# Kernel tuning notes

Measured on AMD Instinct MI355X. Metric: run time of the kernel, lower is better.

Reference implementation:

```python
import jax, jax.numpy as jnp
import numpy as np

N_NODES = 10000
N_EDGES = 160000
IN_DIM = 512
HID = 256
HEADS = 4
OUT_DIM = 512
NEG_SLOPE = 0.2  # PyG GATConv default


def _glorot(key, shape):
    fan_in, fan_out = shape[0], shape[-1]
    lim = jnp.sqrt(6.0 / (fan_in + fan_out))
    return jax.random.uniform(key, shape, jnp.float32, -lim, lim)


def setup_inputs() -> dict:
    key = jax.random.key(0)
    ks = jax.random.split(key, 16)
    x = jax.random.normal(ks[0], (N_NODES, IN_DIM), jnp.float32)
    edge_index = jax.random.randint(ks[1], (2, N_EDGES), 0, N_NODES, jnp.int64)
    # layer 1: GATConv(512 -> 256, heads=4, concat) -> out 1024
    W1 = _glorot(ks[2], (IN_DIM, HEADS * HID))
    att_src1 = _glorot(ks[3], (HEADS, HID))
    att_dst1 = _glorot(ks[4], (HEADS, HID))
    b1 = jnp.zeros((HEADS * HID,), jnp.float32)
    # layer 2: GATConv(1024 -> 256, heads=4, concat) -> out 1024
    W2 = _glorot(ks[5], (HEADS * HID, HEADS * HID))
    att_src2 = _glorot(ks[6], (HEADS, HID))
    att_dst2 = _glorot(ks[7], (HEADS, HID))
    b2 = jnp.zeros((HEADS * HID,), jnp.float32)
    # final fc: 1024 -> 512
    fcW = _glorot(ks[8], (HEADS * HID, OUT_DIM))
    fcb = jnp.zeros((OUT_DIM,), jnp.float32)
    return dict(x=x, edge_index=edge_index, W1=W1, att_src1=att_src1,
                att_dst1=att_dst1, b1=b1, W2=W2, att_src2=att_src2,
                att_dst2=att_dst2, b2=b2, fcW=fcW, fcb=fcb)


def gat_conv(x, src, dst, W, att_src, att_dst, bias):
    # x: [N, F_in]; src/dst: [E] (self-loops already included)
    N = x.shape[0]
    h = (x @ W).reshape(N, HEADS, HID)                       # [N, H, C]
    a_src = jnp.sum(h * att_src, axis=-1)                    # [N, H]
    a_dst = jnp.sum(h * att_dst, axis=-1)                    # [N, H]
    e = jax.nn.leaky_relu(a_src[src] + a_dst[dst], NEG_SLOPE)  # [E, H]
    # numerically stable segment softmax over destination nodes
    m = jax.ops.segment_max(e, dst, num_segments=N)          # [N, H]
    e = jnp.exp(e - m[dst])
    s = jax.ops.segment_sum(e, dst, num_segments=N)          # [N, H]
    alpha = e / (s[dst] + 1e-16)                             # [E, H]
    msg = alpha[:, :, None] * h[src]                         # [E, H, C]
    out = jax.ops.segment_sum(msg, dst, num_segments=N)      # [N, H, C]
    return out.reshape(N, HEADS * HID) + bias


def reference(x, edge_index, W1, att_src1, att_dst1, b1,
              W2, att_src2, att_dst2, b2, fcW, fcb):
    N = x.shape[0]
    loops = jnp.arange(N, dtype=edge_index.dtype)
    src = jnp.concatenate([edge_index[0], loops])  # PyG add_self_loops=True
    dst = jnp.concatenate([edge_index[1], loops])
    h = gat_conv(x, src, dst, W1, att_src1, att_dst1, b1)
    h = jax.nn.relu(h)  # dropout is identity in eval mode
    h = gat_conv(h, src, dst, W2, att_src2, att_dst2, b2)
    h = jax.nn.relu(h)
    return h @ fcW + fcb
```

## Files before the change

### kernel.cpp

```cpp
#include <hip/hip_runtime.h>
#include <hip/hip_bf16.h>

#define NN 10000
#define NE 160000
#define NET 170000
#define IN_DIM 512
#define D1 1024
#define HEADS 4
#define HID 256
#define OUT_DIM 512
#define NEG_SLOPE 0.2f

typedef __attribute__((ext_vector_type(8))) short bf16x8;
typedef __attribute__((ext_vector_type(4))) float f32x4;

__device__ inline float b2f(unsigned short b) {
    union { unsigned u; float f; } x; x.u = ((unsigned)b) << 16; return x.f;
}
__device__ inline unsigned short f2b(float f) {
    union { float f; unsigned u; } x; x.f = f;
    unsigned u = x.u;
    unsigned r = u + 0x7FFFu + ((u >> 16) & 1u);
    return (unsigned short)(r >> 16);
}
__device__ inline float lrelu(float v) { return v > 0.f ? v : NEG_SLOPE * v; }

__device__ inline bool is64(const int* ei32) {
    int acc = 0;
#pragma unroll
    for (int k = 0; k < 16; k++) acc |= ei32[2 * k + 1];
    return acc == 0;
}

__device__ inline void load_edge(const void* ei, bool f64, int e, int& s, int& d) {
    if (f64) {
        const long long* p = (const long long*)ei;
        s = (int)p[e]; d = (int)p[NE + e];
    } else {
        const int* p = (const int*)ei;
        s = p[e]; d = p[NE + e];
    }
}

__global__ void zero_kernel(int* counts, int* cursor) {
    int i = blockIdx.x * blockDim.x + threadIdx.x;
    if (i < NN) { counts[i] = 0; cursor[i] = 0; }
}

__device__ void scan_dev(const int* counts, int* indptr) {
    __shared__ int part[256];
    int t = threadIdx.x;
    int base = t * 40;
    int local[40];
    int sum = 0;
#pragma unroll
    for (int k = 0; k < 40; k++) {
        int i = base + k;
        int c = (i < NN) ? counts[i] : 0;
        local[k] = sum;
        sum += c;
    }
    part[t] = sum;
    __syncthreads();
    for (int off = 1; off < 256; off <<= 1) {
        int v = (t >= off) ? part[t - off] : 0;
        __syncthreads();
        part[t] += v;
        __syncthreads();
    }
    int excl = part[t] - sum;
#pragma unroll
    for (int k = 0; k < 40; k++) {
        int i = base + k;
        if (i < NN) indptr[i] = excl + local[k];
    }
    if (t == 255) indptr[NN] = part[255];
}

__device__ void tpose_tile(const float* __restrict__ in, unsigned short* __restrict__ out,
                           int R, int C, int bx, int by) {
    __shared__ float tile[32][33];
    int tx = threadIdx.x & 31, ty = threadIdx.x >> 5;
    int c = bx * 32 + tx;
#pragma unroll
    for (int r0 = 0; r0 < 32; r0 += 8) {
        int r = by * 32 + ty + r0;
        tile[ty + r0][tx] = in[(size_t)r * C + c];
    }
    __syncthreads();
    int oc = by * 32 + tx;
#pragma unroll
    for (int r0 = 0; r0 < 32; r0 += 8) {
        int orow = bx * 32 + ty + r0;
        out[(size_t)orow * R + oc] = f2b(tile[tx][ty + r0]);
    }
}

#define CVT_NB 5000
#define TP1_NB 512
#define TP2_NB 1024
#define TP3_NB 512
#define CNT_NB 665
__global__ __launch_bounds__(256) void setup_kernel(
    const void* ei, int* counts,
    const float* __restrict__ x, unsigned short* __restrict__ xb,
    const float* __restrict__ W1, unsigned short* __restrict__ W1t,
    const float* __restrict__ W2, unsigned short* __restrict__ W2t,
    const float* __restrict__ fcW, unsigned short* __restrict__ fcWt) {
    int b = blockIdx.x;
    if (b < CVT_NB) {
        int i = b * 256 + threadIdx.x;
        float4 v = reinterpret_cast<const float4*>(x)[i];
        ushort4 o;
        o.x = f2b(v.x); o.y = f2b(v.y); o.z = f2b(v.z); o.w = f2b(v.w);
        reinterpret_cast<ushort4*>(xb)[i] = o;
        return;
    }
    b -= CVT_NB;
    if (b < TP1_NB) { tpose_tile(W1, W1t, IN_DIM, D1, b & 31, b >> 5); return; }
    b -= TP1_NB;
    if (b < TP2_NB) { tpose_tile(W2, W2t, D1, D1, b & 31, b >> 5); return; }
    b -= TP2_NB;
    if (b < TP3_NB) { tpose_tile(fcW, fcWt, D1, OUT_DIM, b & 15, b >> 4); return; }
    b -= TP3_NB;
    int e = b * 256 + threadIdx.x;
    if (e >= NET) return;
    bool f64 = is64((const int*)ei);
    int s, d;
    if (e < NE) load_edge(ei, f64, e, s, d);
    else d = e - NE;
    atomicAdd(&counts[d], 1);
}

template<int TBM, int TBN>
__global__ __launch_bounds__(256) void gemmT(
    const unsigned short* __restrict__ A, const unsigned short* __restrict__ B,
    const float* __restrict__ bias, float* __restrict__ Cf, unsigned short* __restrict__ Cb,
    int M, int N, int K, int NB, int NWG,
    const int* __restrict__ sc_counts, int* __restrict__ sc_indptr) {
    if ((int)blockIdx.x >= NWG) { scan_dev(sc_counts, sc_indptr); return; }
    constexpr int FM = TBM / 32;
    constexpr int FN = TBN / 32;
    constexpr int AISS = TBM / 32;
    constexpr int BISS = TBN / 32;
    constexpr int ABUF = TBM * 64;
    constexpr int BBUF = TBN * 64;
    __shared__ __align__(16) unsigned short As[2 * ABUF];
    __shared__ __align__(16) unsigned short Bs[2 * BBUF];
    int t = threadIdx.x;
    int q = NWG >> 3, r = NWG & 7;
    int xcd = blockIdx.x & 7, jj = blockIdx.x >> 3;
    int wg = (xcd < r ? xcd * (q + 1) : r * (q + 1) + (xcd - r) * q) + jj;
    int row0 = (wg / NB) * TBM, col0 = (wg % NB) * TBN;

    int w = t >> 6, l = t & 63;
    int wr = w >> 1, wc = w & 1;
    f32x4 acc[FM][FN] = {};

    int srow = w * 8 + (l >> 3);
    int scs = ((l & 7) ^ (l >> 3)) * 8;
    const unsigned short* ap[AISS];
    const unsigned short* bp[BISS];
#pragma unroll
    for (int i = 0; i < AISS; i++)
        ap[i] = A + (size_t)min(row0 + i * 32 + srow, M - 1) * K + scs;
#pragma unroll
    for (int i = 0; i < BISS; i++)
        bp[i] = B + (size_t)(col0 + i * 32 + srow) * K + scs;

    int rr = l & 15;
    int rb = (rr & 7) << 4;
    int kb0 = (l >> 4) << 4;
    int c_l = l & 15, r_h = (l >> 4) * 4;

#define GLD(src, dst) __builtin_amdgcn_global_load_lds( \
        (const __attribute__((address_space(1))) void*)(src), \
        (__attribute__((address_space(3))) void*)(dst), 16, 0, 0)

#pragma unroll
    for (int i = 0; i < AISS; i++) { GLD(ap[i], As + i * 2048 + w * 512); ap[i] += 64; }
#pragma unroll
    for (int i = 0; i < BISS; i++) { GLD(bp[i], Bs + i * 2048 + w * 512); bp[i] += 64; }
    __syncthreads();

    int cur = 0;
    for (int k0 = 0; k0 < K; k0 += 64) {
        int nxt = cur ^ 1;
        if (k0 + 64 < K) {
#pragma unroll
            for (int i = 0; i < AISS; i++) {
                GLD(ap[i], As + nxt * ABUF + i * 2048 + w * 512);
                ap[i] += 64;
            }
#pragma unroll
            for (int i = 0; i < BISS; i++) {
                GLD(bp[i], Bs + nxt * BBUF + i * 2048 + w * 512);
                bp[i] += 64;
            }
        }
        const char* Ab = (const char*)(As + cur * ABUF);
        const char* Bb = (const char*)(Bs + cur * BBUF);
#pragma unroll
        for (int ks = 0; ks < 2; ks++) {
            int kb = ((ks << 6) | kb0) ^ rb;
            bf16x8 af[FM], bfv[FN];
#pragma unroll
            for (int mi = 0; mi < FM; mi++)
                af[mi] = *reinterpret_cast<const bf16x8*>(
                    Ab + (wr * (TBM / 2) + mi * 16 + rr) * 128 + kb);
#pragma unroll
            for (int ni = 0; ni < FN; ni++)
                bfv[ni] = *reinterpret_cast<const bf16x8*>(
                    Bb + (wc * (TBN / 2) + ni * 16 + rr) * 128 + kb);
#pragma unroll
            for (int mi = 0; mi < FM; mi++)
#pragma unroll
                for (int ni = 0; ni < FN; ni++)
                    acc[mi][ni] = __builtin_amdgcn_mfma_f32_16x16x32_bf16(
                        af[mi], bfv[ni], acc[mi][ni], 0, 0, 0);
        }
        __syncthreads();
        cur = nxt;
    }
#undef GLD

#pragma unroll
    for (int mi = 0; mi < FM; mi++)
#pragma unroll
        for (int ni = 0; ni < FN; ni++) {
            int gc = col0 + wc * (TBN / 2) + ni * 16 + c_l;
#pragma unroll
            for (int j = 0; j < 4; j++) {
                int gr = row0 + wr * (TBM / 2) + mi * 16 + r_h + j;
                if (gr < M) {
                    float v = acc[mi][ni][j];
                    if (bias) v += bias[gc];
                    if (Cf) Cf[(size_t)gr * N + gc] = v;
                    if (Cb) Cb[(size_t)gr * N + gc] = f2b(v);
                }
            }
        }
}

__global__ __launch_bounds__(256) void att_fill_kernel(
    const unsigned short* __restrict__ hb,
    const float* __restrict__ att_s, const float* __restrict__ att_d,
    float* __restrict__ aS, float* __restrict__ aD,
    const void* ei, const int* __restrict__ indptr,
    int* __restrict__ cursor, int* __restrict__ csr_src, int NATT) {
    if ((int)blockIdx.x >= NATT) {
        int e = ((int)blockIdx.x - NATT) * 256 + threadIdx.x;
        if (e >= NET) return;
        bool f64 = is64((const int*)ei);
        int s, d;
        if (e < NE) load_edge(ei, f64, e, s, d);
        else { s = e - NE; d = s; }
        int pos = indptr[d] + atomicAdd(&cursor[d], 1);
        csr_src[pos] = s;
        return;
    }
    int node = blockIdx.x * 4 + (threadIdx.x >> 6);
    int l = threadIdx.x & 63;
    int head = l >> 4, qq = l & 15;
    const unsigned short* hrow = hb + (size_t)node * D1 + head * HID + qq * 16;
    bf16x8 h0 = *reinterpret_cast<const bf16x8*>(hrow);
    bf16x8 h1 = *reinterpret_cast<const bf16x8*>(hrow + 8);
    const float* asp = att_s + head * HID + qq * 16;
    const float* adp = att_d + head * HID + qq * 16;
    float ps = 0.f, pd = 0.f;
#pragma unroll
    for (int c = 0; c < 8; c++) {
        float hv = b2f((unsigned short)h0[c]);
        float hw = b2f((unsigned short)h1[c]);
        ps += hv * asp[c] + hw * asp[8 + c];
        pd += hv * adp[c] + hw * adp[8 + c];
    }
#pragma unroll
    for (int off = 1; off <= 8; off <<= 1) {
        ps += __shfl_xor(ps, off);
        pd += __shfl_xor(pd, off);
    }
    if (qq == 0) {
        aS[node * HEADS + head] = ps;
        aD[node * HEADS + head] = pd;
    }
}

__global__ __launch_bounds__(256) void agg_kernel(const unsigned short* __restrict__ hb,
                                                  const float* __restrict__ aS,
                                                  const float* __restrict__ aD,
                                                  const int* __restrict__ indptr,
                                                  const int* __restrict__ csr_src,
                                                  const float* __restrict__ bias,
                                                  unsigned short* __restrict__ outb) {
    int node = blockIdx.x * 4 + (threadIdx.x >> 6);
    int l = threadIdx.x & 63;
    int head = l >> 4;
    int beg = indptr[node];
    int deg = indptr[node + 1] - beg;
    float adst = aD[node * HEADS + head];
    const unsigned short* hp = hb + (size_t)l * 16;
    const int* cs = csr_src + beg;
    float acc[16];
#pragma unroll
    for (int c = 0; c < 16; c++) acc[c] = 0.f;
    float esum = 0.f;
    int dm = deg - 1;
    for (int j = 0; j < deg; j += 4) {
        int i0 = j, i1 = min(j + 1, dm), i2 = min(j + 2, dm), i3 = min(j + 3, dm);
        int s0 = cs[i0], s1 = cs[i1], s2 = cs[i2], s3 = cs[i3];
        const unsigned short* r0 = hp + (size_t)s0 * D1;
        const unsigned short* r1 = hp + (size_t)s1 * D1;
        const unsigned short* r2 = hp + (size_t)s2 * D1;
        const unsigned short* r3 = hp + (size_t)s3 * D1;
        bf16x8 r0a = *reinterpret_cast<const bf16x8*>(r0);
        bf16x8 r0b = *reinterpret_cast<const bf16x8*>(r0 + 8);
        bf16x8 r1a = *reinterpret_cast<const bf16x8*>(r1);
        bf16x8 r1b = *reinterpret_cast<const bf16x8*>(r1 + 8);
        bf16x8 r2a = *reinterpret_cast<const bf16x8*>(r2);
        bf16x8 r2b = *reinterpret_cast<const bf16x8*>(r2 + 8);
        bf16x8 r3a = *reinterpret_cast<const bf16x8*>(r3);
        bf16x8 r3b = *reinterpret_cast<const bf16x8*>(r3 + 8);
        float e0 = __expf(lrelu(aS[s0 * HEADS + head] + adst));
        float e1 = (j + 1 <= dm) ? __expf(lrelu(aS[s1 * HEADS + head] + adst)) : 0.f;
        float e2 = (j + 2 <= dm) ? __expf(lrelu(aS[s2 * HEADS + head] + adst)) : 0.f;
        float e3 = (j + 3 <= dm) ? __expf(lrelu(aS[s3 * HEADS + head] + adst)) : 0.f;
        esum += e0 + e1 + e2 + e3;
#pragma unroll
        for (int c = 0; c < 8; c++) {
            acc[c] += e0 * b2f((unsigned short)r0a[c]) + e1 * b2f((unsigned short)r1a[c])
                    + e2 * b2f((unsigned short)r2a[c]) + e3 * b2f((unsigned short)r3a[c]);
            acc[8 + c] += e0 * b2f((unsigned short)r0b[c]) + e1 * b2f((unsigned short)r1b[c])
                        + e2 * b2f((unsigned short)r2b[c]) + e3 * b2f((unsigned short)r3b[c]);
        }
    }
    float inv = 1.f / (esum + 1e-16f);
    const float* bp = bias + l * 16;
    bf16x8 o0, o1;
#pragma unroll
    for (int c = 0; c < 8; c++) {
        o0[c] = (short)f2b(fmaxf(acc[c] * inv + bp[c], 0.f));
        o1[c] = (short)f2b(fmaxf(acc[8 + c] * inv + bp[8 + c], 0.f));
    }
    unsigned short* op = outb + (size_t)node * D1 + l * 16;
    *reinterpret_cast<bf16x8*>(op) = o0;
    *reinterpret_cast<bf16x8*>(op + 8) = o1;
}

extern "C" void kernel_launch(void* const* d_in, const int* in_sizes, int n_in,
                              void* d_out, int out_size, void* d_ws, size_t ws_size,
                              hipStream_t stream) {
    const float* x   = (const float*)d_in[0];
    const void*  ei  = d_in[1];
    const float* W1  = (const float*)d_in[2];
    const float* as1 = (const float*)d_in[3];
    const float* ad1 = (const float*)d_in[4];
    const float* b1  = (const float*)d_in[5];
    const float* W2  = (const float*)d_in[6];
    const float* as2 = (const float*)d_in[7];
    const float* ad2 = (const float*)d_in[8];
    const float* b2  = (const float*)d_in[9];
    const float* fcW = (const float*)d_in[10];
    const float* fcb = (const float*)d_in[11];
    float* out = (float*)d_out;

    char* ws = (char*)d_ws;
    size_t o = 0;
    auto carve = [&](size_t bytes) -> char* {
        char* p = ws + o;
        o = (o + bytes + 255) & ~(size_t)255;
        return p;
    };
    unsigned short* xb   = (unsigned short*)carve((size_t)NN * IN_DIM * 2);
    unsigned short* hb   = (unsigned short*)carve((size_t)NN * D1 * 2);
    unsigned short* x2b  = (unsigned short*)carve((size_t)NN * D1 * 2);
    unsigned short* W1t  = (unsigned short*)carve((size_t)D1 * IN_DIM * 2);
    unsigned short* W2t  = (unsigned short*)carve((size_t)D1 * D1 * 2);
    unsigned short* fcWt = (unsigned short*)carve((size_t)OUT_DIM * D1 * 2);
    float* aS   = (float*)carve((size_t)NN * HEADS * 4);
    float* aD   = (float*)carve((size_t)NN * HEADS * 4);
    int* counts = (int*)carve((size_t)NN * 4);
    int* cursor = (int*)carve((size_t)NN * 4);
    int* indptr = (int*)carve((size_t)(NN + 1) * 4);
    int* csr_src= (int*)carve((size_t)NET * 4);
    (void)ws_size; (void)in_sizes; (void)n_in; (void)out_size;

    const int MB128 = (NN + 127) / 128;
    const int MB64  = (NN + 63) / 64;
    const int G1 = MB128 * (D1 / 64);
    const int GF = MB64 * (OUT_DIM / 64);
    const int NATT = NN / 4;

    zero_kernel<<<(NN + 255) / 256, 256, 0, stream>>>(counts, cursor);
    setup_kernel<<<CVT_NB + TP1_NB + TP2_NB + TP3_NB + CNT_NB, 256, 0, stream>>>(
        ei, counts, x, xb, W1, W1t, W2, W2t, fcW, fcWt);
    gemmT<128, 64><<<G1 + 1, 256, 0, stream>>>(xb, W1t, nullptr, nullptr, hb,
                                               NN, D1, IN_DIM, D1 / 64, G1,
                                               counts, indptr);
    att_fill_kernel<<<NATT + CNT_NB, 256, 0, stream>>>(hb, as1, ad1, aS, aD,
                                                       ei, indptr, cursor, csr_src, NATT);
    agg_kernel<<<NATT, 256, 0, stream>>>(hb, aS, aD, indptr, csr_src, b1, x2b);
    gemmT<128, 64><<<G1, 256, 0, stream>>>(x2b, W2t, nullptr, nullptr, hb,
                                           NN, D1, D1, D1 / 64, G1,
                                           nullptr, nullptr);
    att_fill_kernel<<<NATT, 256, 0, stream>>>(hb, as2, ad2, aS, aD,
                                              ei, indptr, cursor, csr_src, NATT);
    agg_kernel<<<NATT, 256, 0, stream>>>(hb, aS, aD, indptr, csr_src, b2, x2b);
    gemmT<64, 64><<<GF, 256, 0, stream>>>(x2b, fcWt, fcb, out, nullptr,
                                          NN, OUT_DIM, D1, OUT_DIM / 64, GF,
                                          nullptr, nullptr);
}
```

Measured before the change: 229.4 us.

## Triple-buffer GEMM LDS tiles with explicit vmcnt waits and single barrier

Switches the bf16 MFMA GEMM from double to triple buffering in LDS. Two tiles are prefetched ahead, and each iteration waits with a partial s_waitcnt vmcnt, so only the current tile's loads need to have landed, followed by one barrier instead of two __syncthreads. This is meant to hide global load latency better and cut synchronization. In exchange it uses 1.5x the LDS, which can lower occupancy. The hand-coded vmcnt counts assume specific per-thread load counts and only handle AISS+BISS of 4 or 6.

```diff
diff --git a/kernel.cpp b/kernel.cpp
--- a/kernel.cpp
+++ b/kernel.cpp
@@ -145,8 +145,8 @@
     constexpr int BISS = TBN / 32;
     constexpr int ABUF = TBM * 64;
     constexpr int BBUF = TBN * 64;
-    __shared__ __align__(16) unsigned short As[2 * ABUF];
-    __shared__ __align__(16) unsigned short Bs[2 * BBUF];
+    __shared__ __align__(16) unsigned short As[3 * ABUF];
+    __shared__ __align__(16) unsigned short Bs[3 * BBUF];
     int t = threadIdx.x;
     int q = NWG >> 3, r = NWG & 7;
     int xcd = blockIdx.x & 7, jj = blockIdx.x >> 3;
@@ -176,27 +176,33 @@
 #define GLD(src, dst) __builtin_amdgcn_global_load_lds( \
         (const __attribute__((address_space(1))) void*)(src), \
         (__attribute__((address_space(3))) void*)(dst), 16, 0, 0)
-
-#pragma unroll
-    for (int i = 0; i < AISS; i++) { GLD(ap[i], As + i * 2048 + w * 512); ap[i] += 64; }
-#pragma unroll
-    for (int i = 0; i < BISS; i++) { GLD(bp[i], Bs + i * 2048 + w * 512); bp[i] += 64; }
-    __syncthreads();
+#define ISSUE_TILE(buf) do { \
+        _Pragma("unroll") \
+        for (int i = 0; i < AISS; i++) { \
+            GLD(ap[i], As + (buf) * ABUF + i * 2048 + w * 512); ap[i] += 64; } \
+        _Pragma("unroll") \
+        for (int i = 0; i < BISS; i++) { \
+            GLD(bp[i], Bs + (buf) * BBUF + i * 2048 + w * 512); bp[i] += 64; } \
+    } while (0)
+
+    int nt = K >> 6;
+    ISSUE_TILE(0);
+    ISSUE_TILE(1);
 
     int cur = 0;
-    for (int k0 = 0; k0 < K; k0 += 64) {
-        int nxt = cur ^ 1;
-        if (k0 + 64 < K) {
-#pragma unroll
-            for (int i = 0; i < AISS; i++) {
-                GLD(ap[i], As + nxt * ABUF + i * 2048 + w * 512);
-                ap[i] += 64;
-            }
-#pragma unroll
-            for (int i = 0; i < BISS; i++) {
-                GLD(bp[i], Bs + nxt * BBUF + i * 2048 + w * 512);
-                bp[i] += 64;
-            }
+    for (int k = 0; k < nt; k++) {
+        if (k < nt - 1) {
+            if constexpr (AISS + BISS == 6)
+                asm volatile("s_waitcnt vmcnt(6)" ::: "memory");
+            else
+                asm volatile("s_waitcnt vmcnt(4)" ::: "memory");
+        } else {
+            asm volatile("s_waitcnt vmcnt(0)" ::: "memory");
+        }
+        __builtin_amdgcn_s_barrier();
+        if (k + 2 < nt) {
+            int prv = cur - 1; if (prv < 0) prv = 2;
+            ISSUE_TILE(prv);
         }
         const char* Ab = (const char*)(As + cur * ABUF);
         const char* Bb = (const char*)(Bs + cur * BBUF);
@@ -219,9 +225,9 @@
                     acc[mi][ni] = __builtin_amdgcn_mfma_f32_16x16x32_bf16(
                         af[mi], bfv[ni], acc[mi][ni], 0, 0, 0);
         }
-        __syncthreads();
-        cur = nxt;
-    }
+        cur = (cur == 2) ? 0 : cur + 1;
+    }
+#undef ISSUE_TILE
 #undef GLD
 
 #pragma unroll
```

After: 246.6 us. 7.5% more time.
